# Performance work log

Hardware: AMD Instinct MI355X
Metric: run time of the kernel (lower is better)

The kernel has to match this reference:

```python
import jax, jax.numpy as jnp
import numpy as np

B, N, L, C, K, NL, FF = 8, 2048, 2048, 256, 16, 2, 4
RADIUS = 0.12


def setup_inputs() -> dict:
    key = jax.random.key(0)
    ks = jax.random.split(key, 18)
    s = 0.02
    return {
        "q_xyz": jax.random.uniform(ks[0], (B, N, 3), dtype=jnp.float32),
        "q_feat": jax.random.normal(ks[1], (B, N, C), dtype=jnp.float32),
        "kv_xyz": jax.random.uniform(ks[2], (B, L, 3), dtype=jnp.float32),
        "kv_feat": jax.random.normal(ks[3], (B, L, C), dtype=jnp.float32),
        # PointTransformerConv linears (bias=False in PyG)
        "W_src": jax.random.normal(ks[4], (NL, C, C), dtype=jnp.float32) * s,
        "W_dst": jax.random.normal(ks[5], (NL, C, C), dtype=jnp.float32) * s,
        "W_lin": jax.random.normal(ks[6], (NL, C, C), dtype=jnp.float32) * s,
        # attn_nn = Linear(C,C)+ReLU (MLP plain_last=False)
        "W_attn": jax.random.normal(ks[7], (NL, C, C), dtype=jnp.float32) * s,
        "b_attn": jnp.zeros((NL, C), dtype=jnp.float32),
        # FFN
        "W1": jax.random.normal(ks[8], (NL, C, C * FF), dtype=jnp.float32) * s,
        "b1": jnp.zeros((NL, C * FF), dtype=jnp.float32),
        "W2": jax.random.normal(ks[9], (NL, C * FF, C), dtype=jnp.float32) * s,
        "b2": jnp.zeros((NL, C), dtype=jnp.float32),
        # LayerNorms
        "ln1_g": jnp.ones((NL, C), dtype=jnp.float32),
        "ln1_b": jnp.zeros((NL, C), dtype=jnp.float32),
        "ln2_g": jnp.ones((NL, C), dtype=jnp.float32),
        "ln2_b": jnp.zeros((NL, C), dtype=jnp.float32),
    }


def _ln(x, g, b, eps=1e-5):
    mu = x.mean(-1, keepdims=True)
    var = ((x - mu) ** 2).mean(-1, keepdims=True)
    return (x - mu) * jax.lax.rsqrt(var + eps) * g + b


def reference(q_xyz, q_feat, kv_xyz, kv_feat, W_src, W_dst, W_lin, W_attn,
              b_attn, W1, b1, W2, b2, ln1_g, ln1_b, ln2_g, ln2_b):
    # radius ball query: up to K nearest kv points within RADIUS of each query
    d2 = jnp.sum((q_xyz[:, :, None, :] - kv_xyz[:, None, :, :]) ** 2, axis=-1)  # [B,N,L]
    neg, idx = jax.lax.top_k(-d2, K)            # idx: [B,N,K] into L
    valid = (-neg) <= RADIUS * RADIUS           # [B,N,K] in-ball mask
    vmask = valid[..., None].astype(q_feat.dtype)

    gather = jax.vmap(lambda a, i: a[i])        # [B,L,C],[B,N,K] -> [B,N,K,C]
    out = q_feat
    for i in range(NL):
        a_src = kv_feat @ W_src[i]              # [B,L,C]
        a_dst = out @ W_dst[i]                  # [B,N,C]
        v = kv_feat @ W_lin[i]                  # [B,L,C]
        a_src_g = gather(a_src, idx)            # [B,N,K,C]
        v_g = gather(v, idx)                    # [B,N,K,C]
        # attn_nn(lin_dst(x_i) - lin_src(x_j) + delta), delta=0 (ZeroPos)
        alpha = jax.nn.relu(
            jnp.einsum('bnkc,cd->bnkd', a_dst[:, :, None, :] - a_src_g, W_attn[i]) + b_attn[i])
        logits = jnp.where(valid[..., None], alpha, -1e9)
        attn = jax.nn.softmax(logits, axis=2) * vmask   # per-channel softmax over neighbors
        conv = jnp.sum(attn * v_g, axis=2)              # [B,N,C]
        out = _ln(out + conv, ln1_g[i], ln1_b[i])
        h = jax.nn.gelu(out @ W1[i] + b1[i], approximate=False)
        out = _ln(out + h @ W2[i] + b2[i], ln2_g[i], ln2_b[i])
    return out
```

## Files before the change

### kernel.cpp

```cpp
#include <hip/hip_runtime.h>
#include <math.h>

#define BB 8
#define NN 2048
#define LL 2048
#define CC 256
#define KK 16
#define NL 2
#define FF 4

typedef __attribute__((ext_vector_type(8))) short short8v;
typedef __attribute__((ext_vector_type(4))) float f32x4;

__device__ __forceinline__ short f2b(float f) {
    unsigned u = __float_as_uint(f);
    u += 0x7FFFu + ((u >> 16) & 1u);
    return (short)(u >> 16);
}
__device__ __forceinline__ float b2f(short s) {
    return __uint_as_float(((unsigned)(unsigned short)s) << 16);
}
__device__ __forceinline__ float blo(unsigned u) {
    return __uint_as_float(u << 16);
}
__device__ __forceinline__ float bhi(unsigned u) {
    return __uint_as_float(u & 0xffff0000u);
}

__device__ __forceinline__ void g2l16(const void* g, void* l) {
    __builtin_amdgcn_global_load_lds(
        (const __attribute__((address_space(1))) void*)g,
        (__attribute__((address_space(3))) void*)l, 16, 0, 0);
}

__global__ __launch_bounds__(256) void init_k(const float* __restrict__ src,
                                              float* __restrict__ dst,
                                              short* __restrict__ dstb) {
    size_t i = ((size_t)blockIdx.x * 256 + threadIdx.x) * 4;
    float4 v = *reinterpret_cast<const float4*>(src + i);
    *reinterpret_cast<float4*>(dst + i) = v;
    short o[4] = {f2b(v.x), f2b(v.y), f2b(v.z), f2b(v.w)};
    *reinterpret_cast<int2*>(dstb + i) = *reinterpret_cast<int2*>(o);
}

__global__ __launch_bounds__(256) void f2b_k(const float* __restrict__ in,
                                             short* __restrict__ out) {
    size_t i = ((size_t)blockIdx.x * 256 + threadIdx.x) * 4;
    float4 v = *reinterpret_cast<const float4*>(in + i);
    short o[4] = {f2b(v.x), f2b(v.y), f2b(v.z), f2b(v.w)};
    *reinterpret_cast<int2*>(out + i) = *reinterpret_cast<int2*>(o);
}

__global__ __launch_bounds__(256) void tconvB_k(const float* __restrict__ W0,
                                                short* __restrict__ Wt0,
                                                int K, int N,
                                                size_t sin, size_t sout) {
    const float* W = W0 + (size_t)blockIdx.z * sin;
    short* Wt = Wt0 + (size_t)blockIdx.z * sout;
    __shared__ float tile[32][33];
    const int n0 = blockIdx.x * 32, k0 = blockIdx.y * 32;
    const int tx = threadIdx.x & 31, ty = threadIdx.x >> 5;
#pragma unroll
    for (int r = 0; r < 32; r += 8)
        tile[ty + r][tx] = W[(size_t)(k0 + ty + r) * N + n0 + tx];
    __syncthreads();
#pragma unroll
    for (int r = 0; r < 32; r += 8)
        Wt[(size_t)(n0 + ty + r) * K + k0 + tx] = f2b(tile[tx][ty + r]);
}

#define QPB 32
#define CAP 48
__global__ __launch_bounds__(256) void knn_k(const float* __restrict__ qxyz,
                                             const float* __restrict__ kvxyz,
                                             int* __restrict__ idx,
                                             float* __restrict__ valid) {
    __shared__ float4 sxyz[LL];
    __shared__ unsigned long long cpk[QPB][CAP + 1];
    __shared__ int ccnt[QPB];

    const int t   = threadIdx.x;
    const int q   = t >> 3;
    const int sub = t & 7;
    const int b   = blockIdx.x >> 6;
    const int n   = ((blockIdx.x & 63) << 5) + q;

    const float* kb = kvxyz + (size_t)b * LL * 3;
    for (int p = t; p < LL; p += 256)
        sxyz[p] = make_float4(kb[3 * p], kb[3 * p + 1], kb[3 * p + 2], 0.f);
    if (t < QPB) ccnt[t] = 0;
    __syncthreads();

    const size_t qo = (size_t)(b * NN + n) * 3;
    const float qx = qxyz[qo], qy = qxyz[qo + 1], qz = qxyz[qo + 2];
    const float rad2 = (float)(0.12 * 0.12);

    for (int j = sub; j < LL; j += 32) {
        float4 p0 = sxyz[j];
        float4 p1 = sxyz[j + 8];
        float4 p2 = sxyz[j + 16];
        float4 p3 = sxyz[j + 24];
        float x0 = qx - p0.x, y0 = qy - p0.y, z0 = qz - p0.z;
        float x1 = qx - p1.x, y1 = qy - p1.y, z1 = qz - p1.z;
        float x2 = qx - p2.x, y2 = qy - p2.y, z2 = qz - p2.z;
        float x3 = qx - p3.x, y3 = qy - p3.y, z3 = qz - p3.z;
        float d0 = fmaf(x0, x0, fmaf(y0, y0, z0 * z0));
        float d1 = fmaf(x1, x1, fmaf(y1, y1, z1 * z1));
        float d2 = fmaf(x2, x2, fmaf(y2, y2, z2 * z2));
        float d3 = fmaf(x3, x3, fmaf(y3, y3, z3 * z3));
        if (fminf(fminf(d0, d1), fminf(d2, d3)) <= rad2) {
            if (d0 <= rad2) {
                int s = atomicAdd(&ccnt[q], 1);
                if (s < CAP) cpk[q][s] = ((unsigned long long)__float_as_uint(d0) << 32) | (unsigned)(j);
            }
            if (d1 <= rad2) {
                int s = atomicAdd(&ccnt[q], 1);
                if (s < CAP) cpk[q][s] = ((unsigned long long)__float_as_uint(d1) << 32) | (unsigned)(j + 8);
            }
            if (d2 <= rad2) {
                int s = atomicAdd(&ccnt[q], 1);
                if (s < CAP) cpk[q][s] = ((unsigned long long)__float_as_uint(d2) << 32) | (unsigned)(j + 16);
            }
            if (d3 <= rad2) {
                int s = atomicAdd(&ccnt[q], 1);
                if (s < CAP) cpk[q][s] = ((unsigned long long)__float_as_uint(d3) << 32) | (unsigned)(j + 24);
            }
        }
    }
    __syncthreads();

    int c = ccnt[q]; if (c > CAP) c = CAP;
    const size_t o = (size_t)(b * NN + n) * KK;
#pragma unroll 1
    for (int j = sub; j < c; j += 8) {
        const unsigned long long v = cpk[q][j];
        int rank = 0;
#pragma unroll 1
        for (int i = 0; i < c; ++i) rank += (cpk[q][i] < v) ? 1 : 0;
        if (rank < KK) {
            idx[o + rank]   = (int)(v & 0xffffffffu);
            valid[o + rank] = 1.0f;
        }
    }
#pragma unroll
    for (int k = sub; k < KK; k += 8)
        if (k >= c) { idx[o + k] = 0; valid[o + k] = 0.0f; }
}

template <int ACT, int OBF>
__device__ __forceinline__ void mm_body(short* As, short* Bs,
                                        const short* __restrict__ A,
                                        const short* __restrict__ Bt,
                                        const float* __restrict__ bias,
                                        void* __restrict__ Cout,
                                        int N, int Kd, int bx, int by) {
    const int t = threadIdx.x;
    const int lane = t & 63;
    const int wv = t >> 6;
    const int wr = wv >> 1, wc = wv & 1;
    const int lrow = lane & 15;
    const int kc = lane >> 4;
    const int row0 = by * 128;
    const int col0 = bx * 128;

    f32x4 acc[4][4];
#pragma unroll
    for (int m = 0; m < 4; ++m)
#pragma unroll
        for (int n = 0; n < 4; ++n) acc[m][n] = f32x4{0.f, 0.f, 0.f, 0.f};

    const int r0 = t >> 2, cch = t & 3;
    const int scch = cch ^ ((r0 >> 1) & 3);

    for (int k0 = 0; k0 < Kd; k0 += 32) {
        __syncthreads();
        g2l16(A  + (size_t)(row0 + r0) * Kd + k0 + scch * 8,       As + t * 8);
        g2l16(A  + (size_t)(row0 + r0 + 64) * Kd + k0 + scch * 8,  As + 2048 + t * 8);
        g2l16(Bt + (size_t)(col0 + r0) * Kd + k0 + scch * 8,       Bs + t * 8);
        g2l16(Bt + (size_t)(col0 + r0 + 64) * Kd + k0 + scch * 8,  Bs + 2048 + t * 8);
        __syncthreads();
        short8v af[4], bf[4];
#pragma unroll
        for (int m = 0; m < 4; ++m) {
            const int ar = wr * 64 + m * 16 + lrow;
            af[m] = *(const short8v*)(As + ar * 32 + ((kc ^ ((ar >> 1) & 3)) * 8));
        }
#pragma unroll
        for (int n = 0; n < 4; ++n) {
            const int br = wc * 64 + n * 16 + lrow;
            bf[n] = *(const short8v*)(Bs + br * 32 + ((kc ^ ((br >> 1) & 3)) * 8));
        }
#pragma unroll
        for (int m = 0; m < 4; ++m)
#pragma unroll
            for (int n = 0; n < 4; ++n)
                acc[m][n] = __builtin_amdgcn_mfma_f32_16x16x32_bf16(
                    af[m], bf[n], acc[m][n], 0, 0, 0);
    }

    float bcol[4];
#pragma unroll
    for (int n = 0; n < 4; ++n)
        bcol[n] = bias ? bias[col0 + wc * 64 + n * 16 + lrow] : 0.f;

#pragma unroll
    for (int m = 0; m < 4; ++m) {
#pragma unroll
        for (int n = 0; n < 4; ++n) {
            const int col = col0 + wc * 64 + n * 16 + lrow;
#pragma unroll
            for (int r = 0; r < 4; ++r) {
                const int row = row0 + wr * 64 + m * 16 + kc * 4 + r;
                float v = acc[m][n][r] + bcol[n];
                if (ACT == 1) v = 0.5f * v * (1.0f + erff(v * 0.70710678118654752f));
                if (OBF) ((short*)Cout)[(size_t)row * N + col] = f2b(v);
                else     ((float*)Cout)[(size_t)row * N + col] = v;
            }
        }
    }
}

template <int ACT, int OBF>
__global__ __launch_bounds__(256) void mm_k(const short* __restrict__ A,
                                            const short* __restrict__ Bt,
                                            const float* __restrict__ bias,
                                            void* __restrict__ Cout,
                                            int M, int N, int Kd) {
    __shared__ __align__(16) short As[128 * 32];
    __shared__ __align__(16) short Bs[128 * 32];
    mm_body<ACT, OBF>(As, Bs, A, Bt, bias, Cout, N, Kd, blockIdx.x, blockIdx.y);
    (void)M;
}

__global__ __launch_bounds__(256) void wcomb_k(const short* __restrict__ WatT,
                                               const short* __restrict__ Wdst16,
                                               const short* __restrict__ Wsrc16,
                                               short* __restrict__ WcdT,
                                               short* __restrict__ Wsv) {
    __shared__ __align__(16) short As[128 * 32];
    __shared__ __align__(16) short Bs[128 * 32];
    const int z = blockIdx.z, i = z >> 1, sel = z & 1;
    const short* A = WatT + (size_t)i * CC * CC;
    const short* B = (sel ? Wsrc16 : Wdst16) + (size_t)i * CC * CC;
    short* C = sel ? (Wsv + (size_t)i * 2 * CC * CC) : (WcdT + (size_t)i * CC * CC);
    mm_body<0, 1>(As, Bs, A, B, nullptr, C, CC, CC, blockIdx.x, blockIdx.y);
}

#define W2BM 64
__global__ __launch_bounds__(256) void w2ln_k(
    const short* __restrict__ A,
    const short* __restrict__ Bt,
    const float* __restrict__ bias,
    const float* __restrict__ ln_g, const float* __restrict__ ln_b,
    float* __restrict__ out, short* __restrict__ outb) {
    __shared__ __align__(16) short As[W2BM * 32];
    __shared__ __align__(16) short Bs[256 * 32];
    const int t = threadIdx.x;
    const int lane = t & 63;
    const int wv = t >> 6;
    const int lrow = lane & 15;
    const int kc = lane >> 4;
    const int row0 = blockIdx.x * W2BM;
    const int Kd = CC * FF;

    f32x4 acc[16];
#pragma unroll
    for (int n = 0; n < 16; ++n) acc[n] = f32x4{0.f, 0.f, 0.f, 0.f};

    const int r0 = t >> 2, cch = t & 3;
    const int scch = cch ^ ((r0 >> 1) & 3);

    for (int k0 = 0; k0 < Kd; k0 += 32) {
        __syncthreads();
        g2l16(A  + (size_t)(row0 + r0) * Kd + k0 + scch * 8, As + t * 8);
        g2l16(Bt + (size_t)(r0      ) * Kd + k0 + scch * 8, Bs + t * 8);
        g2l16(Bt + (size_t)(r0 +  64) * Kd + k0 + scch * 8, Bs + 2048 + t * 8);
        g2l16(Bt + (size_t)(r0 + 128) * Kd + k0 + scch * 8, Bs + 4096 + t * 8);
        g2l16(Bt + (size_t)(r0 + 192) * Kd + k0 + scch * 8, Bs + 6144 + t * 8);
        __syncthreads();
        const int ar = wv * 16 + lrow;
        short8v af = *(const short8v*)(As + ar * 32 + ((kc ^ ((ar >> 1) & 3)) * 8));
#pragma unroll
        for (int n = 0; n < 16; ++n) {
            const int br = n * 16 + lrow;
            short8v bf = *(const short8v*)(Bs + br * 32 + ((kc ^ ((br >> 1) & 3)) * 8));
            acc[n] = __builtin_amdgcn_mfma_f32_16x16x32_bf16(af, bf, acc[n], 0, 0, 0);
        }
    }

#pragma unroll
    for (int n = 0; n < 16; ++n) {
        const int col = n * 16 + lrow;
        const float bc = bias[col];
#pragma unroll
        for (int r = 0; r < 4; ++r) {
            const int row = row0 + wv * 16 + kc * 4 + r;
            acc[n][r] += bc + out[(size_t)row * CC + col];
        }
    }
#pragma unroll
    for (int r = 0; r < 4; ++r) {
        float s = 0.f;
#pragma unroll
        for (int n = 0; n < 16; ++n) s += acc[n][r];
        s += __shfl_xor(s, 1); s += __shfl_xor(s, 2);
        s += __shfl_xor(s, 4); s += __shfl_xor(s, 8);
        const float mu = s * (1.0f / 256.0f);
        float q = 0.f;
#pragma unroll
        for (int n = 0; n < 16; ++n) {
            const float d = acc[n][r] - mu;
            q = fmaf(d, d, q);
        }
        q += __shfl_xor(q, 1); q += __shfl_xor(q, 2);
        q += __shfl_xor(q, 4); q += __shfl_xor(q, 8);
        const float rstd = rsqrtf(q * (1.0f / 256.0f) + 1e-5f);
        const int row = row0 + wv * 16 + kc * 4 + r;
#pragma unroll
        for (int n = 0; n < 16; ++n) {
            const int col = n * 16 + lrow;
            const float y = (acc[n][r] - mu) * rstd * ln_g[col] + ln_b[col];
            out[(size_t)row * CC + col] = y;
            outb[(size_t)row * CC + col] = f2b(y);
        }
    }
}

#define AQB 4
__global__ __launch_bounds__(256) void attn_ln_k(
    const short* __restrict__ dw, const short* __restrict__ swv,
    const int* __restrict__ idx, const float* __restrict__ valid,
    const float* __restrict__ bat,
    const float* __restrict__ ln_g, const float* __restrict__ ln_b,
    float* __restrict__ out, short* __restrict__ outb) {
    __shared__ int   sidx[AQB * KK];
    __shared__ float sval[AQB * KK];
    __shared__ __align__(16) float sconv[AQB][CC];
    const int t = threadIdx.x;
    const int b   = blockIdx.x & 7;
    const int blk = blockIdx.x >> 3;
    const int bn0 = b * NN + blk * AQB;
    const size_t boff = (size_t)b * LL;

    if (t < AQB * KK) {
        sidx[t] = idx[(size_t)bn0 * KK + t];
        sval[t] = valid[(size_t)bn0 * KK + t];
    }
    __syncthreads();

    const int cp = (t & 127) * 2;
    const int qh = t >> 7;
    const float bias0 = bat[cp], bias1 = bat[cp + 1];
    const unsigned* swvu = (const unsigned*)swv;

#pragma unroll
    for (int qq = 0; qq < 2; ++qq) {
        const int q = qh * 2 + qq;
        const int bn = bn0 + q;
        const unsigned du = *(const unsigned*)(dw + (size_t)bn * CC + cp);
        const float d0 = blo(du) + bias0;
        const float d1 = bhi(du) + bias1;
        float s0 = 0.f, s1 = 0.f, n0 = 0.f, n1 = 0.f;
#pragma unroll
        for (int k = 0; k < KK; ++k) {
            const int j = sidx[q * KK + k];
            const float vv = sval[q * KK + k];
            const unsigned* rp = swvu + (boff + j) * 512;
            const unsigned su = rp[cp >> 1];
            const unsigned vu = rp[128 + (cp >> 1)];
            const float e0 = vv * __expf(fmaxf(d0 - blo(su), 0.f));
            const float e1 = vv * __expf(fmaxf(d1 - bhi(su), 0.f));
            s0 += e0; s1 += e1;
            n0 = fmaf(e0, blo(vu), n0);
            n1 = fmaf(e1, bhi(vu), n1);
        }
        sconv[q][cp]     = (s0 > 0.f) ? n0 / s0 : 0.f;
        sconv[q][cp + 1] = (s1 > 0.f) ? n1 / s1 : 0.f;
    }
    __syncthreads();

    const int lane = t & 63, w = t >> 6;
    float4 gg = *reinterpret_cast<const float4*>(&ln_g[lane * 4]);
    float4 bb = *reinterpret_cast<const float4*>(&ln_b[lane * 4]);
    {
        const int q = w;
        const size_t base = (size_t)(bn0 + q) * CC + lane * 4;
        float4 x = *reinterpret_cast<const float4*>(&out[base]);
        float4 d = *reinterpret_cast<const float4*>(&sconv[q][lane * 4]);
        float v0 = x.x + d.x, v1 = x.y + d.y, v2 = x.z + d.z, v3 = x.w + d.w;
        float s = v0 + v1 + v2 + v3;
#pragma unroll
        for (int o = 32; o > 0; o >>= 1) s += __shfl_xor(s, o);
        const float mu = s * (1.0f / 256.0f);
        const float t0 = v0 - mu, t1 = v1 - mu, t2 = v2 - mu, t3 = v3 - mu;
        float qv = t0 * t0 + t1 * t1 + t2 * t2 + t3 * t3;
#pragma unroll
        for (int o = 32; o > 0; o >>= 1) qv += __shfl_xor(qv, o);
        const float rstd = rsqrtf(qv * (1.0f / 256.0f) + 1e-5f);
        float4 y;
        y.x = t0 * rstd * gg.x + bb.x;
        y.y = t1 * rstd * gg.y + bb.y;
        y.z = t2 * rstd * gg.z + bb.z;
        y.w = t3 * rstd * gg.w + bb.w;
        *reinterpret_cast<float4*>(&out[base]) = y;
        short o4[4] = {f2b(y.x), f2b(y.y), f2b(y.z), f2b(y.w)};
        *reinterpret_cast<int2*>(outb + base) = *reinterpret_cast<int2*>(o4);
    }
}

extern "C" void kernel_launch(void* const* d_in, const int* in_sizes, int n_in,
                              void* d_out, int out_size, void* d_ws, size_t ws_size,
                              hipStream_t stream) {
    const float* q_xyz   = (const float*)d_in[0];
    const float* q_feat  = (const float*)d_in[1];
    const float* kv_xyz  = (const float*)d_in[2];
    const float* kv_feat = (const float*)d_in[3];
    const float* W_src   = (const float*)d_in[4];
    const float* W_dst   = (const float*)d_in[5];
    const float* W_lin   = (const float*)d_in[6];
    const float* W_attn  = (const float*)d_in[7];
    const float* b_attn  = (const float*)d_in[8];
    const float* W1      = (const float*)d_in[9];
    const float* b1      = (const float*)d_in[10];
    const float* W2      = (const float*)d_in[11];
    const float* b2      = (const float*)d_in[12];
    const float* ln1_g   = (const float*)d_in[13];
    const float* ln1_b   = (const float*)d_in[14];
    const float* ln2_g   = (const float*)d_in[15];
    const float* ln2_b   = (const float*)d_in[16];

    float* out = (float*)d_out;
    char* wsb = (char*)d_ws;
    const size_t MB = (size_t)1 << 20;
    int*   idxb   = (int*)(wsb);
    float* validb = (float*)(wsb + 1 * MB);
    short* kvf16  = (short*)(wsb + 2 * MB);
    short* outb16 = (short*)(wsb + 10 * MB);
    short* dw16   = (short*)(wsb + 18 * MB);
    short* swv2   = (short*)(wsb + 26 * MB);
    short* h16    = (short*)(wsb + 58 * MB);
    short* WatT   = (short*)(wsb + 90 * MB);
    short* Wdst16 = (short*)(wsb + 90 * MB + 256 * 1024);
    short* Wsrc16 = (short*)(wsb + 90 * MB + 512 * 1024);
    short* WcdT   = (short*)(wsb + 90 * MB + 768 * 1024);
    short* Wsv    = (short*)(wsb + 91 * MB);
    short* W1T    = (short*)(wsb + 92 * MB);
    short* W2T    = (short*)(wsb + 93 * MB);

    const int M = BB * NN;

    init_k<<<M * CC / (256 * 4), 256, 0, stream>>>(q_feat, out, outb16);
    f2b_k<<<M * CC / (256 * 4), 256, 0, stream>>>(kv_feat, kvf16);
    f2b_k<<<NL * CC * CC / (256 * 4), 256, 0, stream>>>(W_dst, Wdst16);
    f2b_k<<<NL * CC * CC / (256 * 4), 256, 0, stream>>>(W_src, Wsrc16);
    knn_k<<<BB * (NN / QPB), 256, 0, stream>>>(q_xyz, kv_xyz, idxb, validb);

    tconvB_k<<<dim3(8, 8, NL), 256, 0, stream>>>(W_attn, WatT, CC, CC,
                                                 (size_t)CC * CC, (size_t)CC * CC);
    tconvB_k<<<dim3(8, 8, NL), 256, 0, stream>>>(W_lin, Wsv + CC * CC, CC, CC,
                                                 (size_t)CC * CC, (size_t)2 * CC * CC);
    tconvB_k<<<dim3(32, 8, NL), 256, 0, stream>>>(W1, W1T, CC, CC * FF,
                                                  (size_t)CC * CC * FF, (size_t)CC * CC * FF);
    tconvB_k<<<dim3(8, 32, NL), 256, 0, stream>>>(W2, W2T, CC * FF, CC,
                                                  (size_t)CC * CC * FF, (size_t)CC * CC * FF);
    wcomb_k<<<dim3(2, 2, 2 * NL), 256, 0, stream>>>(WatT, Wdst16, Wsrc16, WcdT, Wsv);

    mm_k<0, 1><<<dim3(8, 128), 256, 0, stream>>>(kvf16, Wsv, nullptr, swv2,
                                                 M, 4 * CC, CC);

    for (int i = 0; i < NL; ++i) {
        const size_t oF = (size_t)i * CC * CC * FF;
        const size_t oC = (size_t)i * CC * CC;
        const float* bat = b_attn + (size_t)i * CC;
        const float* b1p = b1 + (size_t)i * CC * FF;
        const float* b2p = b2 + (size_t)i * CC;

        mm_k<0, 1><<<dim3(2, 128), 256, 0, stream>>>(outb16, WcdT + oC, nullptr, dw16, M, CC, CC);

        attn_ln_k<<<M / AQB, 256, 0, stream>>>(dw16, swv2 + (size_t)i * 512,
                                               idxb, validb, bat,
                                               ln1_g + (size_t)i * CC, ln1_b + (size_t)i * CC,
                                               out, outb16);

        mm_k<1, 1><<<dim3(8, 128), 256, 0, stream>>>(outb16, W1T + oF, b1p, h16, M, CC * FF, CC);
        w2ln_k<<<M / W2BM, 256, 0, stream>>>(h16, W2T + oF, b2p,
                                             ln2_g + (size_t)i * CC, ln2_b + (size_t)i * CC,
                                             out, outb16);
    }
    (void)in_sizes; (void)n_in; (void)out_size; (void)ws_size;
}
```

Measured before the change: 284.5 us.

## Double-buffer LDS tiles in GEMM kernels to overlap global loads with MFMA

Converts the shared GEMM body and the W2+LayerNorm kernel from a single LDS buffer to a ping-pong pair. The next K-slice is issued to the alternate buffer before the current slice's MFMAs run, and one barrier per iteration replaces two. This hides global-to-LDS latency behind compute, at the cost of doubled LDS use (up to 40KB in w2ln_k), which may lower occupancy. Correctness depends on g2l16 completing before the trailing barrier.

Measured after the change: 289.9 us. No clear change (+1.9%).

```diff
diff --git a/kernel.cpp b/kernel.cpp
--- a/kernel.cpp
+++ b/kernel.cpp
@@ -171,24 +171,37 @@
 
     const int r0 = t >> 2, cch = t & 3;
     const int scch = cch ^ ((r0 >> 1) & 3);
-
-    for (int k0 = 0; k0 < Kd; k0 += 32) {
-        __syncthreads();
-        g2l16(A  + (size_t)(row0 + r0) * Kd + k0 + scch * 8,       As + t * 8);
-        g2l16(A  + (size_t)(row0 + r0 + 64) * Kd + k0 + scch * 8,  As + 2048 + t * 8);
-        g2l16(Bt + (size_t)(col0 + r0) * Kd + k0 + scch * 8,       Bs + t * 8);
-        g2l16(Bt + (size_t)(col0 + r0 + 64) * Kd + k0 + scch * 8,  Bs + 2048 + t * 8);
-        __syncthreads();
+    const short* Ap0 = A  + (size_t)(row0 + r0) * Kd + scch * 8;
+    const short* Ap1 = A  + (size_t)(row0 + r0 + 64) * Kd + scch * 8;
+    const short* Bp0 = Bt + (size_t)(col0 + r0) * Kd + scch * 8;
+    const short* Bp1 = Bt + (size_t)(col0 + r0 + 64) * Kd + scch * 8;
+
+    auto STAGE = [&](int buf, int k0) {
+        g2l16(Ap0 + k0, As + buf * 4096 + t * 8);
+        g2l16(Ap1 + k0, As + buf * 4096 + 2048 + t * 8);
+        g2l16(Bp0 + k0, Bs + buf * 4096 + t * 8);
+        g2l16(Bp1 + k0, Bs + buf * 4096 + 2048 + t * 8);
+    };
+
+    STAGE(0, 0);
+    __syncthreads();
+
+    const int nt = Kd >> 5;
+    int cur = 0;
+    for (int tt = 0; tt < nt; ++tt) {
+        if (tt + 1 < nt) STAGE(cur ^ 1, (tt + 1) * 32);
+        const short* Ac = As + cur * 4096;
+        const short* Bc = Bs + cur * 4096;
         short8v af[4], bf[4];
 #pragma unroll
         for (int m = 0; m < 4; ++m) {
             const int ar = wr * 64 + m * 16 + lrow;
-            af[m] = *(const short8v*)(As + ar * 32 + ((kc ^ ((ar >> 1) & 3)) * 8));
+            af[m] = *(const short8v*)(Ac + ar * 32 + ((kc ^ ((ar >> 1) & 3)) * 8));
         }
 #pragma unroll
         for (int n = 0; n < 4; ++n) {
             const int br = wc * 64 + n * 16 + lrow;
-            bf[n] = *(const short8v*)(Bs + br * 32 + ((kc ^ ((br >> 1) & 3)) * 8));
+            bf[n] = *(const short8v*)(Bc + br * 32 + ((kc ^ ((br >> 1) & 3)) * 8));
         }
 #pragma unroll
         for (int m = 0; m < 4; ++m)
@@ -196,6 +209,8 @@
             for (int n = 0; n < 4; ++n)
                 acc[m][n] = __builtin_amdgcn_mfma_f32_16x16x32_bf16(
                     af[m], bf[n], acc[m][n], 0, 0, 0);
+        __syncthreads();
+        cur ^= 1;
     }
 
     float bcol[4];
@@ -226,8 +241,8 @@
                                             const float* __restrict__ bias,
                                             void* __restrict__ Cout,
                                             int M, int N, int Kd) {
-    __shared__ __align__(16) short As[128 * 32];
-    __shared__ __align__(16) short Bs[128 * 32];
+    __shared__ __align__(16) short As[2 * 128 * 32];
+    __shared__ __align__(16) short Bs[2 * 128 * 32];
     mm_body<ACT, OBF>(As, Bs, A, Bt, bias, Cout, N, Kd, blockIdx.x, blockIdx.y);
     (void)M;
 }
@@ -237,8 +252,8 @@
                                                const short* __restrict__ Wsrc16,
                                                short* __restrict__ WcdT,
                                                short* __restrict__ Wsv) {
-    __shared__ __align__(16) short As[128 * 32];
-    __shared__ __align__(16) short Bs[128 * 32];
+    __shared__ __align__(16) short As[2 * 128 * 32];
+    __shared__ __align__(16) short Bs[2 * 128 * 32];
     const int z = blockIdx.z, i = z >> 1, sel = z & 1;
     const short* A = WatT + (size_t)i * CC * CC;
     const short* B = (sel ? Wsrc16 : Wdst16) + (size_t)i * CC * CC;
@@ -253,8 +268,8 @@
     const float* __restrict__ bias,
     const float* __restrict__ ln_g, const float* __restrict__ ln_b,
     float* __restrict__ out, short* __restrict__ outb) {
-    __shared__ __align__(16) short As[W2BM * 32];
-    __shared__ __align__(16) short Bs[256 * 32];
+    __shared__ __align__(16) short As[2 * W2BM * 32];
+    __shared__ __align__(16) short Bs[2 * 256 * 32];
     const int t = threadIdx.x;
     const int lane = t & 63;
     const int wv = t >> 6;
@@ -269,23 +284,39 @@
 
     const int r0 = t >> 2, cch = t & 3;
     const int scch = cch ^ ((r0 >> 1) & 3);
-
-    for (int k0 = 0; k0 < Kd; k0 += 32) {
-        __syncthreads();
-        g2l16(A  + (size_t)(row0 + r0) * Kd + k0 + scch * 8, As + t * 8);
-        g2l16(Bt + (size_t)(r0      ) * Kd + k0 + scch * 8, Bs + t * 8);
-        g2l16(Bt + (size_t)(r0 +  64) * Kd + k0 + scch * 8, Bs + 2048 + t * 8);
-        g2l16(Bt + (size_t)(r0 + 128) * Kd + k0 + scch * 8, Bs + 4096 + t * 8);
-        g2l16(Bt + (size_t)(r0 + 192) * Kd + k0 + scch * 8, Bs + 6144 + t * 8);
-        __syncthreads();
+    const short* Ap  = A  + (size_t)(row0 + r0) * Kd + scch * 8;
+    const short* Bq0 = Bt + (size_t)(r0      ) * Kd + scch * 8;
+    const short* Bq1 = Bt + (size_t)(r0 +  64) * Kd + scch * 8;
+    const short* Bq2 = Bt + (size_t)(r0 + 128) * Kd + scch * 8;
+    const short* Bq3 = Bt + (size_t)(r0 + 192) * Kd + scch * 8;
+
+    auto STAGE = [&](int buf, int k0) {
+        g2l16(Ap  + k0, As + buf * 2048 + t * 8);
+        g2l16(Bq0 + k0, Bs + buf * 8192 + t * 8);
+        g2l16(Bq1 + k0, Bs + buf * 8192 + 2048 + t * 8);
+        g2l16(Bq2 + k0, Bs + buf * 8192 + 4096 + t * 8);
+        g2l16(Bq3 + k0, Bs + buf * 8192 + 6144 + t * 8);
+    };
+
+    STAGE(0, 0);
+    __syncthreads();
+
+    const int nt = Kd >> 5;
+    int cur = 0;
+    for (int tt = 0; tt < nt; ++tt) {
+        if (tt + 1 < nt) STAGE(cur ^ 1, (tt + 1) * 32);
+        const short* Ac = As + cur * 2048;
+        const short* Bc = Bs + cur * 8192;
         const int ar = wv * 16 + lrow;
-        short8v af = *(const short8v*)(As + ar * 32 + ((kc ^ ((ar >> 1) & 3)) * 8));
+        short8v af = *(const short8v*)(Ac + ar * 32 + ((kc ^ ((ar >> 1) & 3)) * 8));
 #pragma unroll
         for (int n = 0; n < 16; ++n) {
             const int br = n * 16 + lrow;
-            short8v bf = *(const short8v*)(Bs + br * 32 + ((kc ^ ((br >> 1) & 3)) * 8));
+            short8v bf = *(const short8v*)(Bc + br * 32 + ((kc ^ ((br >> 1) & 3)) * 8));
             acc[n] = __builtin_amdgcn_mfma_f32_16x16x32_bf16(af, bf, acc[n], 0, 0, 0);
         }
+        __syncthreads();
+        cur ^= 1;
     }
 
 #pragma unroll
```

## Halve W2+LayerNorm row tile and split columns across waves

Applied to the files above, without the earlier changes.

The fused W2 GEMM + LayerNorm kernel now uses 32-row tiles instead of 64, and its four waves are arranged as 2 row groups by 2 column halves. Each wave now holds 8 accumulators instead of 16, and the grid has twice as many blocks to fill more CUs. Because each row is now split across two waves, LayerNorm switches to a single-pass sum and sum-of-squares, exchanged through shared memory with an extra barrier. The E[x^2]-mu^2 variance form is less numerically stable, and the full W2 tile is reloaded per block over half as many rows, doubling B-operand traffic. Global address bases are also hoisted out of the K loops in both GEMM kernels.

Measured after the change: 273.2 us. 4.0% less time.

```diff
diff --git a/kernel.cpp b/kernel.cpp
--- a/kernel.cpp
+++ b/kernel.cpp
@@ -171,13 +171,17 @@
 
     const int r0 = t >> 2, cch = t & 3;
     const int scch = cch ^ ((r0 >> 1) & 3);
+    const short* Ap0 = A  + (size_t)(row0 + r0) * Kd + scch * 8;
+    const short* Ap1 = A  + (size_t)(row0 + r0 + 64) * Kd + scch * 8;
+    const short* Bp0 = Bt + (size_t)(col0 + r0) * Kd + scch * 8;
+    const short* Bp1 = Bt + (size_t)(col0 + r0 + 64) * Kd + scch * 8;
 
     for (int k0 = 0; k0 < Kd; k0 += 32) {
         __syncthreads();
-        g2l16(A  + (size_t)(row0 + r0) * Kd + k0 + scch * 8,       As + t * 8);
-        g2l16(A  + (size_t)(row0 + r0 + 64) * Kd + k0 + scch * 8,  As + 2048 + t * 8);
-        g2l16(Bt + (size_t)(col0 + r0) * Kd + k0 + scch * 8,       Bs + t * 8);
-        g2l16(Bt + (size_t)(col0 + r0 + 64) * Kd + k0 + scch * 8,  Bs + 2048 + t * 8);
+        g2l16(Ap0 + k0, As + t * 8);
+        g2l16(Ap1 + k0, As + 2048 + t * 8);
+        g2l16(Bp0 + k0, Bs + t * 8);
+        g2l16(Bp1 + k0, Bs + 2048 + t * 8);
         __syncthreads();
         short8v af[4], bf[4];
 #pragma unroll
@@ -246,7 +250,7 @@
     mm_body<0, 1>(As, Bs, A, B, nullptr, C, CC, CC, blockIdx.x, blockIdx.y);
 }
 
-#define W2BM 64
+#define W2BM 32
 __global__ __launch_bounds__(256) void w2ln_k(
     const short* __restrict__ A,
     const short* __restrict__ Bt,
@@ -255,70 +259,91 @@
     float* __restrict__ out, short* __restrict__ outb) {
     __shared__ __align__(16) short As[W2BM * 32];
     __shared__ __align__(16) short Bs[256 * 32];
+    __shared__ float sstat[4][16][2];
     const int t = threadIdx.x;
     const int lane = t & 63;
     const int wv = t >> 6;
+    const int rg = wv >> 1;
+    const int chl = wv & 1;
     const int lrow = lane & 15;
     const int kc = lane >> 4;
     const int row0 = blockIdx.x * W2BM;
     const int Kd = CC * FF;
 
-    f32x4 acc[16];
-#pragma unroll
-    for (int n = 0; n < 16; ++n) acc[n] = f32x4{0.f, 0.f, 0.f, 0.f};
+    f32x4 acc[8];
+#pragma unroll
+    for (int n = 0; n < 8; ++n) acc[n] = f32x4{0.f, 0.f, 0.f, 0.f};
 
     const int r0 = t >> 2, cch = t & 3;
     const int scch = cch ^ ((r0 >> 1) & 3);
+    const short* Ap  = A  + (size_t)(row0 + (r0 & 31)) * Kd + scch * 8;
+    const short* Bq0 = Bt + (size_t)(r0      ) * Kd + scch * 8;
+    const short* Bq1 = Bt + (size_t)(r0 +  64) * Kd + scch * 8;
+    const short* Bq2 = Bt + (size_t)(r0 + 128) * Kd + scch * 8;
+    const short* Bq3 = Bt + (size_t)(r0 + 192) * Kd + scch * 8;
 
     for (int k0 = 0; k0 < Kd; k0 += 32) {
         __syncthreads();
-        g2l16(A  + (size_t)(row0 + r0) * Kd + k0 + scch * 8, As + t * 8);
-        g2l16(Bt + (size_t)(r0      ) * Kd + k0 + scch * 8, Bs + t * 8);
-        g2l16(Bt + (size_t)(r0 +  64) * Kd + k0 + scch * 8, Bs + 2048 + t * 8);
-        g2l16(Bt + (size_t)(r0 + 128) * Kd + k0 + scch * 8, Bs + 4096 + t * 8);
-        g2l16(Bt + (size_t)(r0 + 192) * Kd + k0 + scch * 8, Bs + 6144 + t * 8);
+        if (t < 128) g2l16(Ap + k0, As + t * 8);
+        g2l16(Bq0 + k0, Bs + t * 8);
+        g2l16(Bq1 + k0, Bs + 2048 + t * 8);
+        g2l16(Bq2 + k0, Bs + 4096 + t * 8);
+        g2l16(Bq3 + k0, Bs + 6144 + t * 8);
         __syncthreads();
-        const int ar = wv * 16 + lrow;
+        const int ar = rg * 16 + lrow;
         short8v af = *(const short8v*)(As + ar * 32 + ((kc ^ ((ar >> 1) & 3)) * 8));
 #pragma unroll
-        for (int n = 0; n < 16; ++n) {
-            const int br = n * 16 + lrow;
+        for (int n = 0; n < 8; ++n) {
+            const int br = chl * 128 + n * 16 + lrow;
             short8v bf = *(const short8v*)(Bs + br * 32 + ((kc ^ ((br >> 1) & 3)) * 8));
             acc[n] = __builtin_amdgcn_mfma_f32_16x16x32_bf16(af, bf, acc[n], 0, 0, 0);
         }
     }
 
 #pragma unroll
-    for (int n = 0; n < 16; ++n) {
-        const int col = n * 16 + lrow;
+    for (int n = 0; n < 8; ++n) {
+        const int col = chl * 128 + n * 16 + lrow;
         const float bc = bias[col];
 #pragma unroll
         for (int r = 0; r < 4; ++r) {
-            const int row = row0 + wv * 16 + kc * 4 + r;
+            const int row = row0 + rg * 16 + kc * 4 + r;
             acc[n][r] += bc + out[(size_t)row * CC + col];
         }
     }
+    float psum[4], psq[4];
 #pragma unroll
     for (int r = 0; r < 4; ++r) {
-        float s = 0.f;
-#pragma unroll
-        for (int n = 0; n < 16; ++n) s += acc[n][r];
+        float s = 0.f, q = 0.f;
+#pragma unroll
+        for (int n = 0; n < 8; ++n) {
+            s += acc[n][r];
+            q = fmaf(acc[n][r], acc[n][r], q);
+        }
         s += __shfl_xor(s, 1); s += __shfl_xor(s, 2);
         s += __shfl_xor(s, 4); s += __shfl_xor(s, 8);
-        const float mu = s * (1.0f / 256.0f);
-        float q = 0.f;
-#pragma unroll
-        for (int n = 0; n < 16; ++n) {
-            const float d = acc[n][r] - mu;
-            q = fmaf(d, d, q);
-        }
         q += __shfl_xor(q, 1); q += __shfl_xor(q, 2);
         q += __shfl_xor(q, 4); q += __shfl_xor(q, 8);
-        const float rstd = rsqrtf(q * (1.0f / 256.0f) + 1e-5f);
-        const int row = row0 + wv * 16 + kc * 4 + r;
-#pragma unroll
-        for (int n = 0; n < 16; ++n) {
-            const int col = n * 16 + lrow;
+        psum[r] = s; psq[r] = q;
+    }
+    if (lrow == 0) {
+#pragma unroll
+        for (int r = 0; r < 4; ++r) {
+            sstat[wv][kc * 4 + r][0] = psum[r];
+            sstat[wv][kc * 4 + r][1] = psq[r];
+        }
+    }
+    __syncthreads();
+#pragma unroll
+    for (int r = 0; r < 4; ++r) {
+        const int lr = kc * 4 + r;
+        const float s = psum[r] + sstat[wv ^ 1][lr][0];
+        const float q = psq[r]  + sstat[wv ^ 1][lr][1];
+        const float mu = s * (1.0f / 256.0f);
+        const float rstd = rsqrtf(fmaxf(q * (1.0f / 256.0f) - mu * mu, 0.f) + 1e-5f);
+        const int row = row0 + rg * 16 + lr;
+#pragma unroll
+        for (int n = 0; n < 8; ++n) {
+            const int col = chl * 128 + n * 16 + lrow;
             const float y = (acc[n][r] - mu) * rstd * ln_g[col] + ln_b[col];
             out[(size_t)row * CC + col] = y;
             outb[(size_t)row * CC + col] = f2b(y);
```
